# Performance work log

Measured on AMD Instinct MI355X. Metric: run time of the kernel, lower is better.

Reference implementation:

```python
import jax, jax.numpy as jnp
import numpy as np

B, S, WIDTH, M = 2, 240, 128, 20
PAD = 16


def setup_inputs() -> dict:
    key = jax.random.key(0)
    ks = jax.random.split(key, 10)
    scale = 1.0 / (WIDTH * WIDTH)
    inp = {
        "x": jax.random.normal(ks[0], (B, S, S, 3), jnp.float32),
        "fc0_w": jax.random.normal(ks[1], (5, WIDTH), jnp.float32) * 0.1,
        "fc0_b": jnp.zeros((WIDTH,), jnp.float32),
        # 5 spectral layers, complex weights stored as [..., 2] = (real, imag)
        "spec_w1": jax.random.uniform(ks[2], (5, WIDTH, WIDTH, M, M, 2), jnp.float32) * scale,
        "spec_w2": jax.random.uniform(ks[3], (5, WIDTH, WIDTH, M, M, 2), jnp.float32) * scale,
        # 5 residual 1x1 convs
        "w_w": jax.random.normal(ks[4], (5, WIDTH, WIDTH), jnp.float32) / np.sqrt(WIDTH),
        "w_b": jnp.zeros((5, WIDTH), jnp.float32),
        "fc1_w": jax.random.normal(ks[5], (WIDTH, WIDTH), jnp.float32) / np.sqrt(WIDTH),
        "fc1_b": jnp.zeros((WIDTH,), jnp.float32),
        # 4 heads (u, v, p, T): width->64->1
        "head1_w": jax.random.normal(ks[6], (4, WIDTH, 64), jnp.float32) / np.sqrt(WIDTH),
        "head1_b": jnp.zeros((4, 64), jnp.float32),
        "head2_w": jax.random.normal(ks[7], (4, 64, 1), jnp.float32) / 8.0,
        "head2_b": jnp.zeros((4, 1), jnp.float32),
    }
    return inp


def _spectral_conv(h, w1, w2):
    # h: (B, C, H, W) real; w1, w2: (C_in, C_out, M, M) complex64
    Hh, Ww = h.shape[-2], h.shape[-1]
    ft = jnp.fft.rfft2(h)  # (B, C, H, W//2+1)
    o1 = jnp.einsum('bixy,ioxy->boxy', ft[:, :, :M, :M], w1)
    o2 = jnp.einsum('bixy,ioxy->boxy', ft[:, :, -M:, :M], w2)
    out_ft = jnp.zeros((h.shape[0], w1.shape[1], Hh, Ww // 2 + 1), jnp.complex64)
    out_ft = out_ft.at[:, :, :M, :M].set(o1).at[:, :, -M:, :M].set(o2)
    return jnp.fft.irfft2(out_ft, s=(Hh, Ww))


def reference(x, fc0_w, fc0_b, spec_w1, spec_w2, w_w, w_b, fc1_w, fc1_b,
              head1_w, head1_b, head2_w, head2_b):
    Bn, sx, sy = x.shape[0], x.shape[1], x.shape[2]
    gx = jnp.broadcast_to(jnp.linspace(0.0, 1.0, sx, dtype=x.dtype)[None, :, None, None], (Bn, sx, sy, 1))
    gy = jnp.broadcast_to(jnp.linspace(0.0, 1.0, sy, dtype=x.dtype)[None, None, :, None], (Bn, sx, sy, 1))
    x1 = jnp.concatenate([x, gx, gy], axis=-1)          # (B, S, S, 5)
    h = x1 @ fc0_w + fc0_b                              # lift -> (B, S, S, width)
    h = jnp.transpose(h, (0, 3, 1, 2))                  # (B, width, S, S)
    h = jnp.pad(h, ((0, 0), (0, 0), (0, PAD), (0, PAD)))
    c1 = spec_w1[..., 0] + 1j * spec_w1[..., 1]
    c2 = spec_w2[..., 0] + 1j * spec_w2[..., 1]
    for i in range(5):
        s = _spectral_conv(h, c1[i], c2[i])
        lin = jnp.einsum('bchw,oc->bohw', h, w_w[i]) + w_b[i][None, :, None, None]
        h = s + lin
        if i < 4:
            h = jax.nn.gelu(h, approximate=False)
    h = h[..., :-PAD, :-PAD]
    h = jnp.transpose(h, (0, 2, 3, 1))                  # (B, S, S, width)
    h = jax.nn.gelu(h @ fc1_w + fc1_b, approximate=False)
    h1 = jax.nn.gelu(jnp.einsum('bhwc,kcd->kbhwd', h, head1_w)
                     + head1_b[:, None, None, None, :], approximate=False)
    out = jnp.einsum('kbhwd,kdo->kbhwo', h1, head2_w) + head2_b[:, None, None, None, :]
    return (out[0], out[1], out[2], out[3])  # u, v, p, T each (B, S, S, 1)
```

## Files before the change

kernel.cpp:

```cpp
#include <hip/hip_runtime.h>
#include <math.h>


#define SZ_H   (2ull*256*256*128)
#define O_HA   0ull
#define O_HB   (O_HA + SZ_H)
#define O_G    (O_HB + SZ_H)
#define SZ_G   (2ull*256*20*128*2)
#define O_FTT  (O_G + SZ_G)
#define SZ_FT  (2ull*40*20*128*2)
#define O_OFT  (O_FTT + SZ_FT)
#define O_EY   (O_OFT + SZ_FT)
#define SZ_EY  (256ull*20*2)
#define O_EX   (O_EY + SZ_EY)
#define SZ_EX  (256ull*40*2)
#define O_EXI  (O_EX + SZ_EX)
#define O_WWT  (O_EXI + SZ_EX)
#define SZ_WWT 81920ull
#define O_PART (O_WWT + SZ_WWT)
#define SZ_PART (8ull*204800*2)

static __device__ __forceinline__ float gelu_f(float v) {
    return 0.5f * v * (1.0f + erff(v * 0.70710678118654752f));
}

__global__ void k_prep(const float* __restrict__ w_w, float* __restrict__ ws) {
    int i = blockIdx.x * 256 + threadIdx.x;
    const float STEP = 6.2831853071795864769f / 256.0f;
    if (i < 5120) {
        int ky = i % 20, y = i / 20;
        int t = (ky * y) & 255;
        float th = t * STEP;
        ws[O_EY + 2*(size_t)i]     = cosf(th);
        ws[O_EY + 2*(size_t)i + 1] = -sinf(th);
    } else if (i < 15360) {
        int m = i - 5120; int j = m % 40, x = m / 40;
        int kx = (j < 20) ? j : (216 + j);
        int t = (kx * x) & 255;
        float th = t * STEP;
        ws[O_EX + 2*(size_t)m]     = cosf(th);
        ws[O_EX + 2*(size_t)m + 1] = -sinf(th);
    } else if (i < 25600) {
        int m = i - 15360; int j = m % 40, x = m / 40;
        int kx = (j < 20) ? j : (216 + j);
        int t = (kx * x) & 255;
        float th = t * STEP;
        ws[O_EXI + 2*(size_t)m]     = cosf(th);
        ws[O_EXI + 2*(size_t)m + 1] = sinf(th);
    } else {
        int m = i - 25600;
        if (m < 81920) {
            int l = m >> 14, r = m & 16383;
            int ic = r >> 7, oc = r & 127;
            ws[O_WWT + m] = w_w[(size_t)l*16384 + oc*128 + ic];
        }
    }
}

__global__ __launch_bounds__(256) void k_fc0(const float* __restrict__ xin,
        const float* __restrict__ w, const float* __restrict__ bv,
        float4* __restrict__ H4) {
    size_t e = (size_t)blockIdx.x * 256 + threadIdx.x;
    int c4 = (int)(e & 31) * 4;
    int y = (int)((e >> 5) & 255);
    int x = (int)((e >> 13) & 255);
    int b = (int)(e >> 21);
    float4 h = make_float4(0.f, 0.f, 0.f, 0.f);
    if (x < 240 && y < 240) {
        const float* xp = xin + (((size_t)(b*240 + x))*240 + y)*3;
        float x0 = xp[0], x1 = xp[1], x2 = xp[2];
        float gx = x*(1.0f/239.0f), gy = y*(1.0f/239.0f);
        float4 w0 = *(const float4*)&w[c4];
        float4 w1 = *(const float4*)&w[128 + c4];
        float4 w2 = *(const float4*)&w[256 + c4];
        float4 w3 = *(const float4*)&w[384 + c4];
        float4 w4 = *(const float4*)&w[512 + c4];
        float4 bb = *(const float4*)&bv[c4];
        h.x = bb.x + x0*w0.x + x1*w1.x + x2*w2.x + gx*w3.x + gy*w4.x;
        h.y = bb.y + x0*w0.y + x1*w1.y + x2*w2.y + gx*w3.y + gy*w4.y;
        h.z = bb.z + x0*w0.z + x1*w1.z + x2*w2.z + gx*w3.z + gy*w4.z;
        h.w = bb.w + x0*w0.w + x1*w1.w + x2*w2.w + gx*w3.w + gy*w4.w;
    }
    H4[e] = h;
}

__global__ __launch_bounds__(256) void k_ydft(const float* __restrict__ H,
        const float* __restrict__ Ey, float2* __restrict__ G) {
    int kh = blockIdx.x & 1;
    int x  = (blockIdx.x >> 1) & 255;
    int b  = blockIdx.x >> 9;
    int c = threadIdx.x & 127;
    int yq = __builtin_amdgcn_readfirstlane((int)(threadIdx.x >> 7));
    int k0 = kh * 10;
    const float* Hrow = H + ((size_t)(b*256 + x)) * 256 * 128;
    float ar[10], ai[10];
    #pragma unroll
    for (int k = 0; k < 10; k++) { ar[k] = 0.f; ai[k] = 0.f; }
    #pragma unroll 2
    for (int i = 0; i < 128; i++) {
        int y = yq*128 + i;
        float v = Hrow[(size_t)y*128 + c];
        const float* e = Ey + (size_t)y*40 + k0*2;
        #pragma unroll
        for (int k = 0; k < 10; k++) {
            ar[k] = fmaf(v, e[2*k],   ar[k]);
            ai[k] = fmaf(v, e[2*k+1], ai[k]);
        }
    }
    __shared__ float red[10][128][2];
    if (yq == 1) {
        #pragma unroll
        for (int k = 0; k < 10; k++) { red[k][c][0] = ar[k]; red[k][c][1] = ai[k]; }
    }
    __syncthreads();
    if (yq == 0) {
        float2* Gp = G + ((size_t)(b*256 + x))*20*128;
        #pragma unroll
        for (int k = 0; k < 10; k++)
            Gp[(k0 + k)*128 + c] = make_float2(ar[k] + red[k][c][0], ai[k] + red[k][c][1]);
    }
}

__global__ __launch_bounds__(256) void k_xdft(const float2* __restrict__ G,
        const float* __restrict__ Ex, float2* __restrict__ ftT) {
    int t = blockIdx.x;
    int ch = t & 3, jq = (t >> 2) & 3, ky = (t >> 4) % 20, b = t / 320;
    int cl = threadIdx.x & 31;
    int xq = threadIdx.x >> 5;
    int c = ch*32 + cl;
    int j0 = jq*10;
    float ar[10], ai[10];
    #pragma unroll
    for (int k = 0; k < 10; k++) { ar[k] = 0.f; ai[k] = 0.f; }
    for (int i = 0; i < 32; i++) {
        int x = xq*32 + i;
        float2 g = G[(((size_t)(b*256 + x))*20 + ky)*128 + c];
        const float2* e2 = (const float2*)(Ex + (size_t)x*80) + j0;
        #pragma unroll
        for (int k = 0; k < 10; k++) {
            float2 e = e2[k];
            ar[k] = fmaf(g.x, e.x, fmaf(-g.y, e.y, ar[k]));
            ai[k] = fmaf(g.x, e.y, fmaf( g.y, e.x, ai[k]));
        }
    }
    #pragma unroll
    for (int k = 0; k < 10; k++) {
        ar[k] += __shfl_xor(ar[k], 32);
        ai[k] += __shfl_xor(ai[k], 32);
    }
    __shared__ float red[3][10][32][2];
    int wid = threadIdx.x >> 6;
    int sub = threadIdx.x & 63;
    if (wid > 0 && sub < 32) {
        #pragma unroll
        for (int k = 0; k < 10; k++) { red[wid-1][k][cl][0] = ar[k]; red[wid-1][k][cl][1] = ai[k]; }
    }
    __syncthreads();
    if (wid == 0 && sub < 32) {
        #pragma unroll
        for (int k = 0; k < 10; k++) {
            float rr = ar[k], ii = ai[k];
            #pragma unroll
            for (int q = 0; q < 3; q++) { rr += red[q][k][cl][0]; ii += red[q][k][cl][1]; }
            ftT[((size_t)c*2 + b)*800 + (size_t)(j0 + k)*20 + ky] = make_float2(rr, ii);
        }
    }
}

__global__ __launch_bounds__(448) void k_modemix(const float2* __restrict__ w1,
        const float2* __restrict__ w2, const float2* __restrict__ ftT,
        float2* __restrict__ outp, int ic_per) {
    int bid = blockIdx.x & 255;
    int icq = blockIdx.x >> 8;
    int oc = bid >> 1;
    int mh = bid & 1;
    int tid = threadIdx.x;
    if (tid >= 400) return;
    int wsel = tid / 200;
    int m = mh*200 + (tid % 200);
    int jk = wsel*400 + m;
    const float2* wb = wsel ? w2 : w1;
    int ic0 = icq * ic_per;
    float ar0=0.f, ai0=0.f, ar1=0.f, ai1=0.f;
    #pragma unroll 8
    for (int i = 0; i < ic_per; i++) {
        int ic = ic0 + i;
        float2 wv = wb[((size_t)(ic*128 + oc))*400 + m];
        float2 f0 = ftT[(size_t)ic*1600 + jk];
        float2 f1 = ftT[(size_t)ic*1600 + 800 + jk];
        ar0 = fmaf(f0.x, wv.x, fmaf(-f0.y, wv.y, ar0));
        ai0 = fmaf(f0.x, wv.y, fmaf( f0.y, wv.x, ai0));
        ar1 = fmaf(f1.x, wv.x, fmaf(-f1.y, wv.y, ar1));
        ai1 = fmaf(f1.x, wv.y, fmaf( f1.y, wv.x, ai1));
    }
    float2* o = outp + (size_t)icq * 204800;
    o[(size_t)jk*128 + oc]         = make_float2(ar0, ai0);
    o[(size_t)(800 + jk)*128 + oc] = make_float2(ar1, ai1);
}

__global__ __launch_bounds__(512) void k_modered(const float2* __restrict__ part,
        float2* __restrict__ oft) {
    int i = blockIdx.x * 512 + threadIdx.x;
    if (i >= 204800) return;
    float2 s = part[i];
    #pragma unroll
    for (int q = 1; q < 8; q++) {
        float2 p = part[(size_t)q*204800 + i];
        s.x += p.x; s.y += p.y;
    }
    oft[i] = s;
}

__global__ __launch_bounds__(256) void k_xidft(const float2* __restrict__ oft,
        const float* __restrict__ Exi, float2* __restrict__ T) {
    int kh = blockIdx.x & 1;
    int x  = (blockIdx.x >> 1) & 255;
    int b  = blockIdx.x >> 9;
    int oc = threadIdx.x & 127;
    int js = __builtin_amdgcn_readfirstlane((int)(threadIdx.x >> 7));
    int k0 = kh * 10;
    float ar[10], ai[10];
    #pragma unroll
    for (int k = 0; k < 10; k++) { ar[k] = 0.f; ai[k] = 0.f; }
    const float2* ob = oft + (size_t)b*800*128;
    for (int j = js*20; j < js*20 + 20; j++) {
        float er = Exi[(size_t)x*80 + 2*j], ei = Exi[(size_t)x*80 + 2*j + 1];
        #pragma unroll
        for (int k = 0; k < 10; k++) {
            float2 o = ob[(size_t)(j*20 + k0 + k)*128 + oc];
            ar[k] = fmaf(o.x, er, fmaf(-o.y, ei, ar[k]));
            ai[k] = fmaf(o.x, ei, fmaf( o.y, er, ai[k]));
        }
    }
    __shared__ float red[10][128][2];
    if (js == 1) {
        #pragma unroll
        for (int k = 0; k < 10; k++) { red[k][oc][0] = ar[k]; red[k][oc][1] = ai[k]; }
    }
    __syncthreads();
    if (js == 0) {
        float2* Tp = T + ((size_t)(b*256 + x))*20*128;
        #pragma unroll
        for (int k = 0; k < 10; k++)
            Tp[(k0 + k)*128 + oc] = make_float2(ar[k] + red[k][oc][0], ai[k] + red[k][oc][1]);
    }
}

__global__ __launch_bounds__(256) void k_spec_lin(const float* __restrict__ H,
        const float2* __restrict__ T, const float* __restrict__ wwT,
        const float* __restrict__ wb, float* __restrict__ Hout, int do_gelu) {
    int yg = blockIdx.x & 3;
    int x  = (blockIdx.x >> 2) & 255;
    int b  = blockIdx.x >> 10;
    int tid = threadIdx.x;
    int lane = tid & 63;
    int wv = __builtin_amdgcn_readfirstlane(tid >> 6);
    int oc0 = wv * 32;
    int y0 = yg * 64;
    __shared__ float hl[64][132];
    const float* Hbase = H + (((size_t)(b*256 + x))*256 + y0)*128;
    #pragma unroll
    for (int it = 0; it < 8; it++) {
        int i = tid + it*256;
        int pi = i >> 5, c4 = (i & 31)*4;
        float4 v = *(const float4*)&Hbase[(size_t)pi*128 + c4];
        *(float4*)&hl[pi][c4] = v;
    }
    __syncthreads();
    float acc[32];
    #pragma unroll
    for (int o = 0; o < 32; o++) acc[o] = 0.f;
    for (int icb = 0; icb < 128; icb += 16) {
        float tvals[16];
        #pragma unroll
        for (int q = 0; q < 4; q++)
            *(float4*)&tvals[q*4] = *(const float4*)&hl[lane][icb + q*4];
        #pragma unroll
        for (int ii = 0; ii < 16; ii++) {
            float t = tvals[ii];
            const float* wr = &wwT[(size_t)(icb + ii)*128 + oc0];
            #pragma unroll
            for (int o4 = 0; o4 < 8; o4++) {
                float4 w = *(const float4*)&wr[o4*4];
                acc[o4*4]   = fmaf(t, w.x, acc[o4*4]);
                acc[o4*4+1] = fmaf(t, w.y, acc[o4*4+1]);
                acc[o4*4+2] = fmaf(t, w.z, acc[o4*4+2]);
                acc[o4*4+3] = fmaf(t, w.w, acc[o4*4+3]);
            }
        }
    }
    float csr[20], csi[20];
    {
        int y = y0 + lane;
        #pragma unroll
        for (int k = 0; k < 20; k++) {
            int t = (k * y) & 255;
            float th = t * (6.2831853071795864769f/256.0f);
            float f = (k == 0 ? 1.0f : 2.0f) * (1.0f/65536.0f);
            csr[k] = f * __cosf(th);
            csi[k] = f * __sinf(th);
        }
    }
    const float2* Tp = T + ((size_t)(b*256 + x))*20*128 + oc0;
    for (int k = 0; k < 20; k++) {
        const float2* tr = Tp + (size_t)k*128;
        float cr = csr[k], ci = csi[k];
        #pragma unroll
        for (int o = 0; o < 32; o++) {
            float2 tv = tr[o];
            acc[o] = fmaf(tv.x, cr, fmaf(-tv.y, ci, acc[o]));
        }
    }
    __syncthreads();
    const float* bp = &wb[oc0];
    #pragma unroll
    for (int o4 = 0; o4 < 8; o4++) {
        float4 r;
        r.x = acc[o4*4]   + bp[o4*4];
        r.y = acc[o4*4+1] + bp[o4*4+1];
        r.z = acc[o4*4+2] + bp[o4*4+2];
        r.w = acc[o4*4+3] + bp[o4*4+3];
        if (do_gelu) { r.x = gelu_f(r.x); r.y = gelu_f(r.y); r.z = gelu_f(r.z); r.w = gelu_f(r.w); }
        *(float4*)&hl[lane][oc0 + o4*4] = r;
    }
    __syncthreads();
    float* Obase = Hout + (((size_t)(b*256 + x))*256 + y0)*128;
    #pragma unroll
    for (int it = 0; it < 32; it++) {
        int i = tid + it*256;
        int pi = i >> 7, c = i & 127;
        Obase[(size_t)pi*128 + c] = hl[pi][c];
    }
}

__global__ __launch_bounds__(512) void k_tail(const float* __restrict__ H,
        const float* __restrict__ fc1_w, const float* __restrict__ fc1_b,
        const float* __restrict__ h1w, const float* __restrict__ h1b,
        const float* __restrict__ h2w, const float* __restrict__ h2b,
        float* __restrict__ out) {
    int tid = threadIdx.x;
    int lane = tid & 63;
    int wv = __builtin_amdgcn_readfirstlane(tid >> 6);
    int p0 = blockIdx.x * 64;
    __shared__ float smem[64*132];
    __shared__ float red[4][64];
    float (*hl)[132] = (float (*)[132])smem;
    #pragma unroll
    for (int it = 0; it < 4; it++) {
        int i = tid + it*512;
        int pi = i >> 5, c4 = (i & 31)*4;
        int p = p0 + pi;
        int bb = p / 57600, r = p % 57600;
        int xx = r / 240, yy = r % 240;
        float4 v = *(const float4*)&H[(((size_t)(bb*256 + xx))*256 + yy)*128 + c4];
        *(float4*)&hl[pi][c4] = v;
    }
    __syncthreads();
    int oc0 = wv * 16;
    float acc[16];
    #pragma unroll
    for (int o = 0; o < 16; o++) acc[o] = 0.f;
    for (int icb = 0; icb < 128; icb += 16) {
        float tvals[16];
        #pragma unroll
        for (int q = 0; q < 4; q++)
            *(float4*)&tvals[q*4] = *(const float4*)&hl[lane][icb + q*4];
        #pragma unroll
        for (int ii = 0; ii < 16; ii++) {
            float t = tvals[ii];
            const float* wr = &fc1_w[(size_t)(icb + ii)*128 + oc0];
            #pragma unroll
            for (int o4 = 0; o4 < 4; o4++) {
                float4 w = *(const float4*)&wr[o4*4];
                acc[o4*4]   = fmaf(t, w.x, acc[o4*4]);
                acc[o4*4+1] = fmaf(t, w.y, acc[o4*4+1]);
                acc[o4*4+2] = fmaf(t, w.z, acc[o4*4+2]);
                acc[o4*4+3] = fmaf(t, w.w, acc[o4*4+3]);
            }
        }
    }
    __syncthreads();
    #pragma unroll
    for (int o4 = 0; o4 < 4; o4++) {
        float4 bb = *(const float4*)&fc1_b[oc0 + o4*4];
        float4 r;
        r.x = gelu_f(acc[o4*4]   + bb.x);
        r.y = gelu_f(acc[o4*4+1] + bb.y);
        r.z = gelu_f(acc[o4*4+2] + bb.z);
        r.w = gelu_f(acc[o4*4+3] + bb.w);
        *(float4*)&hl[lane][oc0 + o4*4] = r;
    }
    __syncthreads();
    int k    = wv >> 1;
    int half = wv & 1;
    int d0 = half * 32;
    float a2[32];
    #pragma unroll
    for (int d = 0; d < 32; d++) a2[d] = 0.f;
    const float* wk = h1w + (size_t)k*8192 + d0;
    for (int cb = 0; cb < 128; cb += 8) {
        float tvals[8];
        *(float4*)&tvals[0] = *(const float4*)&hl[lane][cb];
        *(float4*)&tvals[4] = *(const float4*)&hl[lane][cb + 4];
        #pragma unroll
        for (int cc = 0; cc < 8; cc++) {
            float t = tvals[cc];
            const float* wr = &wk[(cb + cc)*64];
            #pragma unroll
            for (int d4 = 0; d4 < 8; d4++) {
                float4 w = *(const float4*)&wr[d4*4];
                a2[d4*4]   = fmaf(t, w.x, a2[d4*4]);
                a2[d4*4+1] = fmaf(t, w.y, a2[d4*4+1]);
                a2[d4*4+2] = fmaf(t, w.z, a2[d4*4+2]);
                a2[d4*4+3] = fmaf(t, w.w, a2[d4*4+3]);
            }
        }
    }
    const float* b1 = &h1b[k*64 + d0];
    const float* w2 = &h2w[k*64 + d0];
    float ph = 0.f;
    #pragma unroll
    for (int d = 0; d < 32; d++)
        ph += gelu_f(a2[d] + b1[d]) * w2[d];
    if (half == 1) red[k][lane] = ph;
    __syncthreads();
    if (half == 0)
        out[(size_t)k*115200 + p0 + lane] = ph + red[k][lane] + h2b[k];
}

extern "C" void kernel_launch(void* const* d_in, const int* in_sizes, int n_in,
                              void* d_out, int out_size, void* d_ws, size_t ws_size,
                              hipStream_t stream) {
    const float* x       = (const float*)d_in[0];
    const float* fc0_w   = (const float*)d_in[1];
    const float* fc0_b   = (const float*)d_in[2];
    const float* spec_w1 = (const float*)d_in[3];
    const float* spec_w2 = (const float*)d_in[4];
    const float* w_w     = (const float*)d_in[5];
    const float* w_b     = (const float*)d_in[6];
    const float* fc1_w   = (const float*)d_in[7];
    const float* fc1_b   = (const float*)d_in[8];
    const float* head1_w = (const float*)d_in[9];
    const float* head1_b = (const float*)d_in[10];
    const float* head2_w = (const float*)d_in[11];
    const float* head2_b = (const float*)d_in[12];
    float* ws = (float*)d_ws;
    float* out = (float*)d_out;

    int split = ws_size >= (size_t)(O_PART + SZ_PART) * 4 ? 1 : 0;

    k_prep<<<420, 256, 0, stream>>>(w_w, ws);
    k_fc0<<<16384, 256, 0, stream>>>(x, fc0_w, fc0_b, (float4*)(ws + O_HA));

    float* cur = ws + O_HA;
    float* nxt = ws + O_HB;
    float2* G    = (float2*)(ws + O_G);
    float2* ftT  = (float2*)(ws + O_FTT);
    float2* oft  = (float2*)(ws + O_OFT);
    float2* part = (float2*)(ws + O_PART);

    for (int l = 0; l < 5; l++) {
        k_ydft<<<1024, 256, 0, stream>>>(cur, ws + O_EY, G);
        k_xdft<<<640, 256, 0, stream>>>(G, ws + O_EX, ftT);
        const float2* w1l = (const float2*)(spec_w1 + (size_t)l*13107200);
        const float2* w2l = (const float2*)(spec_w2 + (size_t)l*13107200);
        if (split) {
            k_modemix<<<2048, 448, 0, stream>>>(w1l, w2l, ftT, part, 16);
            k_modered<<<400, 512, 0, stream>>>(part, oft);
        } else {
            k_modemix<<<256, 448, 0, stream>>>(w1l, w2l, ftT, oft, 128);
        }
        k_xidft<<<1024, 256, 0, stream>>>(oft, ws + O_EXI, G);
        k_spec_lin<<<2048, 256, 0, stream>>>(cur, G, ws + O_WWT + (size_t)l*16384,
                                             w_b + l*128, nxt, (l < 4) ? 1 : 0);
        float* t = cur; cur = nxt; nxt = t;
    }
    k_tail<<<1800, 512, 0, stream>>>(cur, fc1_w, fc1_b, head1_w, head1_b,
                                     head2_w, head2_b, out);
}
```

Baseline: 1.726 ms.

## Approximate GELU erf, enlarge spectral-linear and tail tiles to 128 pixels

Replaces erff in GELU with the Abramowitz–Stegun polynomial approximation using a fast reciprocal and exp. k_spec_lin now processes 128 y-rows per 512-thread block so each weight load is shared across two waves. k_tail handles 128 pixels per block, with each thread computing two pixels in fc1 and all 64 head hidden units, which removes the cross-wave reduction. This trades some erf accuracy (about 1e-7 absolute error) and higher register pressure for fewer transcendental instructions and fewer redundant weight loads.

```diff
diff --git a/kernel.cpp b/kernel.cpp
--- a/kernel.cpp
+++ b/kernel.cpp
@@ -21,7 +21,15 @@
 #define SZ_PART (8ull*204800*2)
 
 static __device__ __forceinline__ float gelu_f(float v) {
-    return 0.5f * v * (1.0f + erff(v * 0.70710678118654752f));
+    float z  = v * 0.70710678118654752f;
+    float az = fabsf(z);
+    float t  = __builtin_amdgcn_rcpf(fmaf(0.3275911f, az, 1.0f));
+    float p  = fmaf(fmaf(fmaf(fmaf(1.061405429f, t, -1.453152027f), t,
+                    1.421413741f), t, -0.284496736f), t, 0.254829592f);
+    float e  = __expf(-z * z);
+    float er = fmaf(-p * t, e, 1.0f);
+    er = copysignf(er, z);
+    return 0.5f * v * (1.0f + er);
 }
 
 __global__ void k_prep(const float* __restrict__ w_w, float* __restrict__ ws) {
@@ -246,27 +254,29 @@
     }
 }
 
-__global__ __launch_bounds__(256) void k_spec_lin(const float* __restrict__ H,
+__global__ __launch_bounds__(512) void k_spec_lin(const float* __restrict__ H,
         const float2* __restrict__ T, const float* __restrict__ wwT,
         const float* __restrict__ wb, float* __restrict__ Hout, int do_gelu) {
-    int yg = blockIdx.x & 3;
-    int x  = (blockIdx.x >> 2) & 255;
-    int b  = blockIdx.x >> 10;
+    int yg = blockIdx.x & 1;
+    int x  = (blockIdx.x >> 1) & 255;
+    int b  = blockIdx.x >> 9;
     int tid = threadIdx.x;
     int lane = tid & 63;
     int wv = __builtin_amdgcn_readfirstlane(tid >> 6);
-    int oc0 = wv * 32;
-    int y0 = yg * 64;
-    __shared__ float hl[64][132];
+    int og = wv & 3, yh = wv >> 2;
+    int oc0 = og * 32;
+    int y0 = yg * 128;
+    __shared__ __align__(16) float hl[128][132];
     const float* Hbase = H + (((size_t)(b*256 + x))*256 + y0)*128;
     #pragma unroll
     for (int it = 0; it < 8; it++) {
-        int i = tid + it*256;
+        int i = tid + it*512;
         int pi = i >> 5, c4 = (i & 31)*4;
         float4 v = *(const float4*)&Hbase[(size_t)pi*128 + c4];
         *(float4*)&hl[pi][c4] = v;
     }
     __syncthreads();
+    int yrow = yh*64 + lane;
     float acc[32];
     #pragma unroll
     for (int o = 0; o < 32; o++) acc[o] = 0.f;
@@ -274,7 +284,7 @@
         float tvals[16];
         #pragma unroll
         for (int q = 0; q < 4; q++)
-            *(float4*)&tvals[q*4] = *(const float4*)&hl[lane][icb + q*4];
+            *(float4*)&tvals[q*4] = *(const float4*)&hl[yrow][icb + q*4];
         #pragma unroll
         for (int ii = 0; ii < 16; ii++) {
             float t = tvals[ii];
@@ -291,7 +301,7 @@
     }
     float csr[20], csi[20];
     {
-        int y = y0 + lane;
+        int y = y0 + yrow;
         #pragma unroll
         for (int k = 0; k < 20; k++) {
             int t = (k * y) & 255;
@@ -321,13 +331,13 @@
         r.z = acc[o4*4+2] + bp[o4*4+2];
         r.w = acc[o4*4+3] + bp[o4*4+3];
         if (do_gelu) { r.x = gelu_f(r.x); r.y = gelu_f(r.y); r.z = gelu_f(r.z); r.w = gelu_f(r.w); }
-        *(float4*)&hl[lane][oc0 + o4*4] = r;
+        *(float4*)&hl[yrow][oc0 + o4*4] = r;
     }
     __syncthreads();
     float* Obase = Hout + (((size_t)(b*256 + x))*256 + y0)*128;
     #pragma unroll
     for (int it = 0; it < 32; it++) {
-        int i = tid + it*256;
+        int i = tid + it*512;
         int pi = i >> 7, c = i & 127;
         Obase[(size_t)pi*128 + c] = hl[pi][c];
     }
@@ -341,12 +351,10 @@
     int tid = threadIdx.x;
     int lane = tid & 63;
     int wv = __builtin_amdgcn_readfirstlane(tid >> 6);
-    int p0 = blockIdx.x * 64;
-    __shared__ float smem[64*132];
-    __shared__ float red[4][64];
-    float (*hl)[132] = (float (*)[132])smem;
-    #pragma unroll
-    for (int it = 0; it < 4; it++) {
+    int p0 = blockIdx.x * 128;
+    __shared__ __align__(16) float hl[128][132];
+    #pragma unroll
+    for (int it = 0; it < 8; it++) {
         int i = tid + it*512;
         int pi = i >> 5, c4 = (i & 31)*4;
         int p = p0 + pi;
@@ -357,58 +365,67 @@
     }
     __syncthreads();
     int oc0 = wv * 16;
-    float acc[16];
-    #pragma unroll
-    for (int o = 0; o < 16; o++) acc[o] = 0.f;
-    for (int icb = 0; icb < 128; icb += 16) {
-        float tvals[16];
-        #pragma unroll
-        for (int q = 0; q < 4; q++)
-            *(float4*)&tvals[q*4] = *(const float4*)&hl[lane][icb + q*4];
-        #pragma unroll
-        for (int ii = 0; ii < 16; ii++) {
-            float t = tvals[ii];
+    float acc0[16], acc1[16];
+    #pragma unroll
+    for (int o = 0; o < 16; o++) { acc0[o] = 0.f; acc1[o] = 0.f; }
+    for (int icb = 0; icb < 128; icb += 8) {
+        float tv0[8], tv1[8];
+        *(float4*)&tv0[0] = *(const float4*)&hl[lane][icb];
+        *(float4*)&tv0[4] = *(const float4*)&hl[lane][icb + 4];
+        *(float4*)&tv1[0] = *(const float4*)&hl[lane + 64][icb];
+        *(float4*)&tv1[4] = *(const float4*)&hl[lane + 64][icb + 4];
+        #pragma unroll
+        for (int ii = 0; ii < 8; ii++) {
+            float t0 = tv0[ii], t1 = tv1[ii];
             const float* wr = &fc1_w[(size_t)(icb + ii)*128 + oc0];
             #pragma unroll
             for (int o4 = 0; o4 < 4; o4++) {
                 float4 w = *(const float4*)&wr[o4*4];
-                acc[o4*4]   = fmaf(t, w.x, acc[o4*4]);
-                acc[o4*4+1] = fmaf(t, w.y, acc[o4*4+1]);
-                acc[o4*4+2] = fmaf(t, w.z, acc[o4*4+2]);
-                acc[o4*4+3] = fmaf(t, w.w, acc[o4*4+3]);
+                acc0[o4*4]   = fmaf(t0, w.x, acc0[o4*4]);
+                acc0[o4*4+1] = fmaf(t0, w.y, acc0[o4*4+1]);
+                acc0[o4*4+2] = fmaf(t0, w.z, acc0[o4*4+2]);
+                acc0[o4*4+3] = fmaf(t0, w.w, acc0[o4*4+3]);
+                acc1[o4*4]   = fmaf(t1, w.x, acc1[o4*4]);
+                acc1[o4*4+1] = fmaf(t1, w.y, acc1[o4*4+1]);
+                acc1[o4*4+2] = fmaf(t1, w.z, acc1[o4*4+2]);
+                acc1[o4*4+3] = fmaf(t1, w.w, acc1[o4*4+3]);
             }
         }
     }
     __syncthreads();
     #pragma unroll
     for (int o4 = 0; o4 < 4; o4++) {
-        float4 bb = *(const float4*)&fc1_b[oc0 + o4*4];
-        float4 r;
-        r.x = gelu_f(acc[o4*4]   + bb.x);
-        r.y = gelu_f(acc[o4*4+1] + bb.y);
-        r.z = gelu_f(acc[o4*4+2] + bb.z);
-        r.w = gelu_f(acc[o4*4+3] + bb.w);
-        *(float4*)&hl[lane][oc0 + o4*4] = r;
-    }
-    __syncthreads();
-    int k    = wv >> 1;
-    int half = wv & 1;
-    int d0 = half * 32;
-    float a2[32];
-    #pragma unroll
-    for (int d = 0; d < 32; d++) a2[d] = 0.f;
-    const float* wk = h1w + (size_t)k*8192 + d0;
+        float4 b4 = *(const float4*)&fc1_b[oc0 + o4*4];
+        float4 r0, r1;
+        r0.x = gelu_f(acc0[o4*4]   + b4.x);
+        r0.y = gelu_f(acc0[o4*4+1] + b4.y);
+        r0.z = gelu_f(acc0[o4*4+2] + b4.z);
+        r0.w = gelu_f(acc0[o4*4+3] + b4.w);
+        r1.x = gelu_f(acc1[o4*4]   + b4.x);
+        r1.y = gelu_f(acc1[o4*4+1] + b4.y);
+        r1.z = gelu_f(acc1[o4*4+2] + b4.z);
+        r1.w = gelu_f(acc1[o4*4+3] + b4.w);
+        *(float4*)&hl[lane][oc0 + o4*4]      = r0;
+        *(float4*)&hl[lane + 64][oc0 + o4*4] = r1;
+    }
+    __syncthreads();
+    int k  = wv & 3, ph = wv >> 2;
+    int px = ph*64 + lane;
+    float a2[64];
+    #pragma unroll
+    for (int d = 0; d < 64; d++) a2[d] = 0.f;
+    const float* wk = h1w + (size_t)k*8192;
     for (int cb = 0; cb < 128; cb += 8) {
-        float tvals[8];
-        *(float4*)&tvals[0] = *(const float4*)&hl[lane][cb];
-        *(float4*)&tvals[4] = *(const float4*)&hl[lane][cb + 4];
+        float tv[8];
+        *(float4*)&tv[0] = *(const float4*)&hl[px][cb];
+        *(float4*)&tv[4] = *(const float4*)&hl[px][cb + 4];
         #pragma unroll
         for (int cc = 0; cc < 8; cc++) {
-            float t = tvals[cc];
-            const float* wr = &wk[(cb + cc)*64];
+            float t = tv[cc];
+            const float4* wp = (const float4*)&wk[(size_t)(cb + cc)*64];
             #pragma unroll
-            for (int d4 = 0; d4 < 8; d4++) {
-                float4 w = *(const float4*)&wr[d4*4];
+            for (int d4 = 0; d4 < 16; d4++) {
+                float4 w = wp[d4];
                 a2[d4*4]   = fmaf(t, w.x, a2[d4*4]);
                 a2[d4*4+1] = fmaf(t, w.y, a2[d4*4+1]);
                 a2[d4*4+2] = fmaf(t, w.z, a2[d4*4+2]);
@@ -416,16 +433,13 @@
             }
         }
     }
-    const float* b1 = &h1b[k*64 + d0];
-    const float* w2 = &h2w[k*64 + d0];
-    float ph = 0.f;
-    #pragma unroll
-    for (int d = 0; d < 32; d++)
-        ph += gelu_f(a2[d] + b1[d]) * w2[d];
-    if (half == 1) red[k][lane] = ph;
-    __syncthreads();
-    if (half == 0)
-        out[(size_t)k*115200 + p0 + lane] = ph + red[k][lane] + h2b[k];
+    float s = 0.f;
+    const float* b1 = &h1b[k*64];
+    const float* w2 = &h2w[k*64];
+    #pragma unroll
+    for (int d = 0; d < 64; d++)
+        s += gelu_f(a2[d] + b1[d]) * w2[d];
+    out[(size_t)k*115200 + p0 + px] = s + h2b[k];
 }
 
 extern "C" void kernel_launch(void* const* d_in, const int* in_sizes, int n_in,
@@ -471,10 +485,10 @@
             k_modemix<<<256, 448, 0, stream>>>(w1l, w2l, ftT, oft, 128);
         }
         k_xidft<<<1024, 256, 0, stream>>>(oft, ws + O_EXI, G);
-        k_spec_lin<<<2048, 256, 0, stream>>>(cur, G, ws + O_WWT + (size_t)l*16384,
+        k_spec_lin<<<1024, 512, 0, stream>>>(cur, G, ws + O_WWT + (size_t)l*16384,
                                              w_b + l*128, nxt, (l < 4) ? 1 : 0);
         float* t = cur; cur = nxt; nxt = t;
     }
-    k_tail<<<1800, 512, 0, stream>>>(cur, fc1_w, fc1_b, head1_w, head1_b,
-                                     head2_w, head2_b, out);
-}
+    k_tail<<<900, 512, 0, stream>>>(cur, fc1_w, fc1_b, head1_w, head1_b,
+                                    head2_w, head2_b, out);
+}
```

Result: no change. 1.759 ms (+1.9%).
